# Optimization experiments

Hardware: AMD Instinct MI355X
Metric: run time of the kernel (lower is better)

The kernel has to match this reference:

```python
import jax, jax.numpy as jnp
import numpy as np

B, S, C, DG, DO, G = 128, 512, 256, 256, 4, 10
ZONEOUT = 0.1  # ZoneOutCell eval-mode: h = z*h_prev + (1-z)*h_new


def setup_inputs() -> dict:
    key = jax.random.key(0)
    ks = jax.random.split(key, 12)
    def w(k, shape, fan):
        return jax.random.normal(k, shape, jnp.float32) / np.sqrt(fan).astype(np.float32)
    return {
        "encoder_output": jax.random.normal(ks[0], (B, S, C), jnp.float32),
        "target_prosody": jax.random.normal(ks[1], (B, S, DO), jnp.float32),
        "snt_durations": jax.random.randint(ks[2], (B, S), 0, 10),
        "W_pre": w(ks[3], (DO, DO), DO), "b_pre": jnp.zeros((DO,), jnp.float32),
        "Wih0": w(ks[4], (3 * DG, C + DO), C + DO), "Whh0": w(ks[5], (3 * DG, DG), DG),
        "bih0": jnp.zeros((3 * DG,), jnp.float32), "bhh0": jnp.zeros((3 * DG,), jnp.float32),
        "Wih1": w(ks[6], (3 * DG, DG), DG), "Whh1": w(ks[7], (3 * DG, DG), DG),
        "bih1": jnp.zeros((3 * DG,), jnp.float32), "bhh1": jnp.zeros((3 * DG,), jnp.float32),
        "W_pi": w(ks[8], (G, C + DG), C + DG), "b_pi": jnp.zeros((G,), jnp.float32),
        "W_sigma": w(ks[9], (DO * G, C + DG), C + DG), "b_sigma": jnp.zeros((DO * G,), jnp.float32),
        "W_mu": w(ks[10], (DO * G, C + DG), C + DG), "b_mu": jnp.zeros((DO * G,), jnp.float32),
    }


def _gru_cell(x, h, Wih, Whh, bih, bhh):
    # torch.nn.GRUCell math, wrapped in eval-mode ZoneOut
    gi = x @ Wih.T + bih
    gh = h @ Whh.T + bhh
    ir, iz, inn = jnp.split(gi, 3, axis=-1)
    hr, hz, hn = jnp.split(gh, 3, axis=-1)
    r = jax.nn.sigmoid(ir + hr)
    z = jax.nn.sigmoid(iz + hz)
    n = jnp.tanh(inn + r * hn)
    h_new = (1.0 - z) * n + z * h
    return ZONEOUT * h + (1.0 - ZONEOUT) * h_new


def _forward(encoder_output, target_prosody, W_pre, b_pre, Wih0, Whh0, bih0, bhh0,
             Wih1, Whh1, bih1, bhh1, W_pi, b_pi, W_sigma, b_sigma, W_mu, b_mu):
    tgt = jax.lax.stop_gradient(target_prosody)  # teacher-forced prev_out is detached
    # prev_out at step t is go_frame (zeros) then target[:, t-1]
    prev = jnp.concatenate([jnp.zeros((B, 1, DO), tgt.dtype), tgt[:, :-1, :]], axis=1)
    prenet = prev @ W_pre.T + b_pre                       # (B,S,DO)
    xs = jnp.concatenate([encoder_output, prenet], -1)    # (B,S,C+DO)

    def step(carry, x_t):
        h0, h1 = carry
        h0 = _gru_cell(x_t, h0, Wih0, Whh0, bih0, bhh0)
        h1 = _gru_cell(h0, h1, Wih1, Whh1, bih1, bhh1)
        return (h0, h1), h1

    init = (jnp.zeros((B, DG), xs.dtype), jnp.zeros((B, DG), xs.dtype))
    _, H = jax.lax.scan(step, init, jnp.swapaxes(xs, 0, 1))  # (S,B,DG)
    H = jnp.swapaxes(H, 0, 1)                                # (B,S,DG)

    hcs = jnp.concatenate([H, encoder_output], axis=-1)      # (B,S,DG+C)
    pi = jax.nn.softmax(hcs @ W_pi.T + b_pi, axis=-1)                       # (B,S,G)
    sigma = (jax.nn.elu(hcs @ W_sigma.T + b_sigma) + 1.0).reshape(B, S, G, DO)
    mu = (hcs @ W_mu.T + b_mu).reshape(B, S, G, DO)
    return tgt, pi, sigma, mu


def reference(encoder_output, target_prosody, snt_durations, W_pre, b_pre, Wih0, Whh0,
              bih0, bhh0, Wih1, Whh1, bih1, bhh1, W_pi, b_pi, W_sigma, b_sigma, W_mu, b_mu):
    outs, pi, sigma, mu = _forward(encoder_output, target_prosody, W_pre, b_pre,
                                   Wih0, Whh0, bih0, bhh0, Wih1, Whh1, bih1, bhh1,
                                   W_pi, b_pi, W_sigma, b_sigma, W_mu, b_mu)
    # make_src_mask: True where padded (index >= number of non-zero durations)
    snt_nums = jnp.sum(snt_durations > 0, axis=-1)           # (B,)
    src_snt_mask = jnp.arange(S)[None, :] >= snt_nums[:, None]
    return outs, pi, sigma, mu, src_snt_mask
```

## Files before the change

kernel.cpp:

```cpp
#include <hip/hip_runtime.h>
#include <hip/hip_bf16.h>
#include <stdint.h>

#define B_   128
#define S_   512
#define C_   256
#define DG_  256

#define OFF_PI   262144
#define OFF_SIG  917504
#define OFF_MU   3538944
#define OFF_MASK 6160384

typedef __hip_bfloat16 bf16;
typedef __bf16 bf16x8 __attribute__((ext_vector_type(8)));
typedef float  f32x4  __attribute__((ext_vector_type(4)));
typedef unsigned int u32;
typedef unsigned int u32x4 __attribute__((ext_vector_type(4)));

__device__ __align__(16) bf16  gWmain[768*256];
__device__ __align__(16) bf16  gWHH0 [768*256];
__device__ __align__(16) bf16  gWIH1 [768*256];
__device__ __align__(16) bf16  gWHH1 [768*256];
__device__ __align__(16) bf16  gWcat [96*512];
__device__ __align__(16) float gWtail[768*4];
__device__ __align__(16) float gSm   [3200];
__device__ __align__(16) bf16  gHbuf [B_*S_*DG_];
__device__ __align__(16) bf16  gH0   [B_*S_*DG_];
__device__ __align__(16) float gGi0  [50331648];
__device__ __align__(16) float gGi1  [50331648];
__device__ __align__(16) float gPn   [65536*4];

#define SM_WPRE 0
#define SM_BPRE 16
#define SM_BIH0 20
#define SM_BHH0 788
#define SM_BIH1 1556
#define SM_BHH1 2324
#define SM_BPI  3092
#define SM_BSIG 3102
#define SM_BMU  3142

__device__ __forceinline__ bf16  f2b(float x){ return __float2bfloat16(x); }
__device__ __forceinline__ unsigned short b2u(bf16 x){
    union { bf16 b; unsigned short u; } c; c.b = x; return c.u;
}
__device__ __forceinline__ float sigm(float x){ return 1.f/(1.f + __expf(-x)); }
__device__ __forceinline__ float tanhfast(float x){ return 1.f - 2.f/(__expf(2.f*x) + 1.f); }
__device__ __forceinline__ float rcp_fast(float x){
    float r; asm("v_rcp_f32 %0, %1" : "=v"(r) : "v"(x)); return r;
}
__device__ __forceinline__ u32 cvtpk_bf16(float lo, float hi){
    u32 r; asm("v_cvt_pk_bf16_f32 %0, %1, %2" : "=v"(r) : "v"(lo), "v"(hi)); return r;
}
__device__ __forceinline__ f32x4 mfma16(bf16x8 a, bf16x8 b, f32x4 c){
    return __builtin_amdgcn_mfma_f32_16x16x32_bf16(a, b, c, 0, 0, 0);
}
__device__ __forceinline__ bf16x8 u2b(u32x4 x){
    union { u32x4 u; bf16x8 b; } c; c.u = x; return c.b;
}
__device__ __forceinline__ bf16x8 cvt8(const float* f){
    float4 a = *reinterpret_cast<const float4*>(f);
    float4 c = *reinterpret_cast<const float4*>(f + 4);
    bf16 o[8] = { f2b(a.x),f2b(a.y),f2b(a.z),f2b(a.w),
                  f2b(c.x),f2b(c.y),f2b(c.z),f2b(c.w) };
    return *reinterpret_cast<bf16x8*>(o);
}

#define IN_N0 199680
#define IN_N1 396288
#define IN_N2 592896
#define IN_N3 789504
#define IN_N4 838656
#define IN_N5 841838
#define IN_N6 1103982
__global__ __launch_bounds__(256) void k_ingest(
    const float* __restrict__ Wih0, const float* __restrict__ Whh0,
    const float* __restrict__ Wih1, const float* __restrict__ Whh1,
    const float* __restrict__ Wpi, const float* __restrict__ Wsig,
    const float* __restrict__ Wmu,
    const float* __restrict__ Wpre, const float* __restrict__ bpre,
    const float* __restrict__ bih0, const float* __restrict__ bhh0,
    const float* __restrict__ bih1, const float* __restrict__ bhh1,
    const float* __restrict__ bpi, const float* __restrict__ bsig,
    const float* __restrict__ bmu, const float* __restrict__ tgt)
{
    int j = blockIdx.x*256 + threadIdx.x;
    if (j < IN_N0){
        int r = j/260, c = j - r*260;
        float v = Wih0[j];
        if (c < 256) gWmain[r*256 + c] = f2b(v);
        else         gWtail[r*4 + (c-256)] = v;
    } else if (j < IN_N1){
        int k = j - IN_N0; gWHH0[k] = f2b(Whh0[k]);
    } else if (j < IN_N2){
        int k = j - IN_N1; gWIH1[k] = f2b(Wih1[k]);
    } else if (j < IN_N3){
        int k = j - IN_N2; gWHH1[k] = f2b(Whh1[k]);
    } else if (j < IN_N4){
        int k = j - IN_N3; int r = k >> 9, c = k & 511;
        float v = 0.f;
        if      (r < 10) v = Wpi[r*512 + c];
        else if (r < 50) v = Wsig[(r-10)*512 + c];
        else if (r < 90) v = Wmu[(r-50)*512 + c];
        gWcat[k] = f2b(v);
    } else if (j < IN_N5){
        int k = j - IN_N4;
        float v;
        if      (k < 16)   v = Wpre[k];
        else if (k < 20)   v = bpre[k-16];
        else if (k < 788)  v = bih0[k-20];
        else if (k < 1556) v = bhh0[k-788];
        else if (k < 2324) v = bih1[k-1556];
        else if (k < 3092) v = bhh1[k-2324];
        else if (k < 3102) v = bpi[k-3092];
        else if (k < 3142) v = bsig[k-3102];
        else               v = bmu[k-3142];
        gSm[k] = v;
    } else if (j < IN_N6){
        int k = j - IN_N5, m = k>>2, jj = k&3, tq = m&511;
        float acc = bpre[jj];
        if (tq){
            const float* pv = tgt + (size_t)(m-1)*4;
            #pragma unroll
            for (int q=0;q<4;q++) acc += Wpre[jj*4+q]*pv[q];
        }
        gPn[m*4+jj] = acc;
    }
}

__global__ __launch_bounds__(256) void k_gi0(const float* __restrict__ enc)
{
    const int tid = threadIdx.x, w = tid>>6, lane = tid&63;
    const int col = lane&15, quad = lane>>4;
    const int m0 = blockIdx.x*64 + w*16;

    bf16x8 aF[8];
    #pragma unroll
    for (int kt=0; kt<8; kt++)
        aF[kt] = cvt8(enc + (size_t)(m0+col)*256 + kt*32 + quad*8);

    float4 pnr[4];
    #pragma unroll
    for (int r=0; r<4; r++)
        pnr[r] = *reinterpret_cast<const float4*>(gPn + (size_t)(m0 + quad*4 + r)*4);
    const int mrow = m0 + quad*4;

    for (int nt=0; nt<48; nt++){
        const int n = nt*16 + col;
        f32x4 acc = {0.f,0.f,0.f,0.f};
        #pragma unroll
        for (int kt=0; kt<8; kt++){
            bf16x8 bW = *reinterpret_cast<const bf16x8*>(gWmain + (size_t)n*256 + kt*32 + quad*8);
            acc = mfma16(aF[kt], bW, acc);
        }
        float4 wt = ((const float4*)gWtail)[n];
        float  bi = gSm[SM_BIH0 + n] + ((n < 512) ? gSm[SM_BHH0 + n] : 0.f);
        #pragma unroll
        for (int r=0; r<4; r++){
            int m = mrow + r; int bq = m>>9, tq = m&511;
            float v = acc[r] + bi + wt.x*pnr[r].x + wt.y*pnr[r].y
                              + wt.z*pnr[r].z + wt.w*pnr[r].w;
            gGi0[((size_t)tq*128 + bq)*768 + n] = v;
        }
    }
}

__global__ __launch_bounds__(256) void k_gi1()
{
    const int tid = threadIdx.x, w = tid>>6, lane = tid&63;
    const int col = lane&15, quad = lane>>4;
    const int m0 = blockIdx.x*64 + w*16;

    bf16x8 aF[8];
    #pragma unroll
    for (int kt=0; kt<8; kt++)
        aF[kt] = *reinterpret_cast<const bf16x8*>(gH0 + (size_t)(m0+col)*256 + kt*32 + quad*8);

    for (int nt=0; nt<48; nt++){
        const int n = nt*16 + col;
        f32x4 acc = {0.f,0.f,0.f,0.f};
        #pragma unroll
        for (int kt=0; kt<8; kt++){
            bf16x8 bW = *reinterpret_cast<const bf16x8*>(gWIH1 + (size_t)n*256 + kt*32 + quad*8);
            acc = mfma16(aF[kt], bW, acc);
        }
        float bi = gSm[SM_BIH1 + n] + ((n < 512) ? gSm[SM_BHH1 + n] : 0.f);
        #pragma unroll
        for (int r=0; r<4; r++)
            gGi1[((size_t)(m0 + quad*4 + r))*768 + n] = acc[r] + bi;
    }
}

__global__ __launch_bounds__(256, 1) void k_rec(int layer)
{
    __shared__ bf16 hv[2][4][272];

    const bf16*  __restrict__ W  = layer ? gWHH1 : gWHH0;
    const float* __restrict__ gi = layer ? gGi1  : gGi0;
    const int smOff = layer ? SM_BHH1 : SM_BHH0;
    bf16* __restrict__ hout = layer ? gHbuf : gH0;

    const int tid = threadIdx.x, w = tid>>6, lane = tid&63;
    const int col = lane&15, quad = lane>>4;
    const int bg4 = blockIdx.x*4;
    const int c4 = col&3, qsel = col>>2;

    for (int i=tid; i<2*4*272; i+=256) (&hv[0][0][0])[i] = f2b(0.f);

    u32x4 wA[8][8];
    #pragma unroll
    for (int j=0;j<8;j++){
        const int qi = j/3, g = j - qi*3;
        const bf16* Wr = W + ((size_t)(g*256 + (4*w+qi)*16 + col))*256;
        #pragma unroll
        for (int kt=0;kt<8;kt++){
            wA[j][kt] = *reinterpret_cast<const u32x4*>(Wr + kt*32 + quad*8);
            asm volatile("" : "+a"(wA[j][kt]));
        }
    }
    u32x4 wV[4][8];
    #pragma unroll
    for (int j=0;j<4;j++){
        const int jj = 8+j, qi = jj/3, g = jj - qi*3;
        const bf16* Wr = W + ((size_t)(g*256 + (4*w+qi)*16 + col))*256;
        #pragma unroll
        for (int kt=0;kt<8;kt++){
            wV[j][kt] = *reinterpret_cast<const u32x4*>(Wr + kt*32 + quad*8);
            asm volatile("" : "+v"(wV[j][kt]));
        }
    }

    const int q = 4*w + qsel;
    const int d = q*16 + quad*4;
    float4 bhn = *reinterpret_cast<const float4*>(&gSm[smOff + 512 + d]);
    const float* gib = gi + (size_t)(bg4 + c4)*768 + d;
    bf16* hop; size_t hstep;
    if (layer){ hop = hout + ((size_t)(bg4+c4)*512)*256 + d; hstep = 256; }
    else      { hop = hout + (size_t)(bg4+c4)*256 + d;       hstep = 128*256; }
    float hreg[4] = {0.f,0.f,0.f,0.f};

    float4 gr = *reinterpret_cast<const float4*>(gib);
    float4 gz = *reinterpret_cast<const float4*>(gib + 256);
    float4 gn = *reinterpret_cast<const float4*>(gib + 512);

    __syncthreads();

    #pragma unroll 1
    for (int t=0; t<S_; t++){
        float4 pr, pz, pnx;
        if (t+1 < S_){
            const float* gq = gib + (size_t)(t+1)*98304;
            pr  = *reinterpret_cast<const float4*>(gq);
            pz  = *reinterpret_cast<const float4*>(gq + 256);
            pnx = *reinterpret_cast<const float4*>(gq + 512);
        }

        f32x4 acc[12];
        #pragma unroll
        for (int j=0;j<12;j++) acc[j] = f32x4{0.f,0.f,0.f,0.f};
        asm volatile("s_nop 2" :::);

        const bf16* hrow = &hv[t&1][c4][0];
        #pragma unroll
        for (int kt=0;kt<8;kt++){
            u32x4 hbu = *reinterpret_cast<const u32x4*>(hrow + kt*32 + quad*8);
            #pragma unroll
            for (int j=0;j<8;j++)
                asm volatile("v_mfma_f32_16x16x32_bf16 %0, %1, %2, %0"
                             : "+v"(acc[j]) : "a"(wA[j][kt]), "v"(hbu));
            bf16x8 hbb = u2b(hbu);
            #pragma unroll
            for (int j=0;j<4;j++)
                acc[8+j] = mfma16(u2b(wV[j][kt]), hbb, acc[8+j]);
        }
        asm volatile("s_nop 7\n\ts_nop 7" :::);

        f32x4 aR = (qsel==0) ? acc[0] : (qsel==1) ? acc[3] : (qsel==2) ? acc[6] : acc[9];
        f32x4 aZ = (qsel==0) ? acc[1] : (qsel==1) ? acc[4] : (qsel==2) ? acc[7] : acc[10];
        f32x4 aN = (qsel==0) ? acc[2] : (qsel==1) ? acc[5] : (qsel==2) ? acc[8] : acc[11];

        float hp[4];
        #pragma unroll
        for (int r=0;r<4;r++){
            float rr = rcp_fast(1.f + __expf(-(((const float*)&gr)[r] + aR[r])));
            float zz = rcp_fast(1.f + __expf(-(((const float*)&gz)[r] + aZ[r])));
            float xn = ((const float*)&gn)[r] + rr*(aN[r] + ((const float*)&bhn)[r]);
            float nn = 1.f - 2.f*rcp_fast(__expf(2.f*xn) + 1.f);
            float h  = hreg[r];
            float v  = 0.1f*h + 0.9f*((1.f-zz)*nn + zz*h);
            hreg[r] = v; hp[r] = v;
        }

        uint2 u;
        u.x = cvtpk_bf16(hp[0], hp[1]);
        u.y = cvtpk_bf16(hp[2], hp[3]);
        *reinterpret_cast<uint2*>(&hv[(t&1)^1][c4][d]) = u;
        *reinterpret_cast<uint2*>(hop) = u;  hop += hstep;

        gr = pr; gz = pz; gn = pnx;

        asm volatile("s_waitcnt lgkmcnt(0)" ::: "memory");
        __builtin_amdgcn_sched_barrier(0);
        __builtin_amdgcn_s_barrier();
        __builtin_amdgcn_sched_barrier(0);
    }
}

__global__ __launch_bounds__(256) void k_proj(
    const float* __restrict__ enc, float* __restrict__ dout)
{
    __shared__ float st[128][100];
    const int tid = threadIdx.x, w = tid>>6, lane = tid&63;
    const int col = lane&15, quad = lane>>4;
    const int Mb = blockIdx.x*128;
    const int M0 = Mb + w*32;

    f32x4 acc[2][6];
    #pragma unroll
    for (int mt=0; mt<2; mt++)
        #pragma unroll
        for (int nt=0; nt<6; nt++) acc[mt][nt] = f32x4{0.f,0.f,0.f,0.f};

    #pragma unroll
    for (int kt=0; kt<16; kt++){
        bf16x8 a0, a1;
        if (kt < 8){
            a0 = *reinterpret_cast<const bf16x8*>(gHbuf + (size_t)(M0 +      col)*DG_ + kt*32 + quad*8);
            a1 = *reinterpret_cast<const bf16x8*>(gHbuf + (size_t)(M0 + 16 + col)*DG_ + kt*32 + quad*8);
        } else {
            a0 = cvt8(enc + (size_t)(M0 +      col)*C_ + (kt-8)*32 + quad*8);
            a1 = cvt8(enc + (size_t)(M0 + 16 + col)*C_ + (kt-8)*32 + quad*8);
        }
        #pragma unroll
        for (int nt=0; nt<6; nt++){
            bf16x8 b = *reinterpret_cast<const bf16x8*>(gWcat + (size_t)(nt*16 + col)*512 + kt*32 + quad*8);
            acc[0][nt] = mfma16(a0, b, acc[0][nt]);
            acc[1][nt] = mfma16(a1, b, acc[1][nt]);
        }
    }
    #pragma unroll
    for (int nt=0; nt<6; nt++)
        #pragma unroll
        for (int mt=0; mt<2; mt++)
            #pragma unroll
            for (int r=0; r<4; r++)
                st[w*32 + mt*16 + quad*4 + r][nt*16 + col] = acc[mt][nt][r];
    __syncthreads();

    if (tid < 128){
        const float* v = st[tid];
        const size_t m = (size_t)Mb + tid;
        float x[10], mx = -1e30f;
        #pragma unroll
        for (int g=0; g<10; g++){ x[g] = v[g] + gSm[SM_BPI+g]; mx = fmaxf(mx, x[g]); }
        float sum = 0.f;
        #pragma unroll
        for (int g=0; g<10; g++){ x[g] = __expf(x[g]-mx); sum += x[g]; }
        float inv = 1.f/sum;
        #pragma unroll
        for (int g=0; g<10; g++)
            dout[OFF_PI + m*10 + g] = x[g]*inv;
        #pragma unroll
        for (int i=0; i<40; i++){
            float s = v[10+i] + gSm[SM_BSIG+i];
            dout[OFF_SIG + m*40 + i] = (s > 0.f) ? (s + 1.f) : __expf(s);
        }
        #pragma unroll
        for (int i=0; i<40; i++)
            dout[OFF_MU + m*40 + i] = v[50+i] + gSm[SM_BMU+i];
    }
}

__global__ __launch_bounds__(256) void k_misc(const float* __restrict__ tgt,
    const int* __restrict__ dur, float* __restrict__ dout)
{
    if (blockIdx.x < 256){
        int i = blockIdx.x*256 + threadIdx.x;
        ((float4*)dout)[i] = ((const float4*)tgt)[i];
    } else {
        __shared__ int red[256];
        int b = blockIdx.x - 256;
        int c = 0;
        for (int s = threadIdx.x; s < S_; s += 256) c += (dur[b*S_ + s] > 0) ? 1 : 0;
        red[threadIdx.x] = c;
        __syncthreads();
        for (int off=128; off>0; off>>=1){
            if (threadIdx.x < off) red[threadIdx.x] += red[threadIdx.x+off];
            __syncthreads();
        }
        int snt = red[0];
        for (int s = threadIdx.x; s < S_; s += 256)
            dout[OFF_MASK + (size_t)b*S_ + s] = (s >= snt) ? 1.f : 0.f;
    }
}

extern "C" void kernel_launch(void* const* d_in, const int* in_sizes, int n_in,
                              void* d_out, int out_size, void* d_ws, size_t ws_size,
                              hipStream_t stream)
{
    (void)d_ws; (void)ws_size;
    const float* enc  = (const float*)d_in[0];
    const float* tgt  = (const float*)d_in[1];
    const int*   dur  = (const int*)  d_in[2];
    const float* Wpre = (const float*)d_in[3];
    const float* bpre = (const float*)d_in[4];
    const float* Wih0 = (const float*)d_in[5];
    const float* Whh0 = (const float*)d_in[6];
    const float* bih0 = (const float*)d_in[7];
    const float* bhh0 = (const float*)d_in[8];
    const float* Wih1 = (const float*)d_in[9];
    const float* Whh1 = (const float*)d_in[10];
    const float* bih1 = (const float*)d_in[11];
    const float* bhh1 = (const float*)d_in[12];
    const float* Wpi  = (const float*)d_in[13];
    const float* bpi  = (const float*)d_in[14];
    const float* Wsig = (const float*)d_in[15];
    const float* bsig = (const float*)d_in[16];
    const float* Wmu  = (const float*)d_in[17];
    const float* bmu  = (const float*)d_in[18];
    float* dout = (float*)d_out;

    hipLaunchKernelGGL(k_ingest, dim3(4313), dim3(256), 0, stream,
                       Wih0, Whh0, Wih1, Whh1, Wpi, Wsig, Wmu,
                       Wpre, bpre, bih0, bhh0, bih1, bhh1, bpi, bsig, bmu, tgt);
    hipLaunchKernelGGL(k_gi0,  dim3(1024), dim3(256), 0, stream, enc);
    hipLaunchKernelGGL(k_rec,  dim3(32),   dim3(256), 0, stream, 0);
    hipLaunchKernelGGL(k_gi1,  dim3(1024), dim3(256), 0, stream);
    hipLaunchKernelGGL(k_rec,  dim3(32),   dim3(256), 0, stream, 1);
    hipLaunchKernelGGL(k_proj, dim3(512),  dim3(256), 0, stream, enc, dout);
    hipLaunchKernelGGL(k_misc, dim3(384),  dim3(256), 0, stream, tgt, dur, dout);
}
```

Baseline: 1.982 ms.

## Split recurrent GRU kernel across 8 waves with LDS-staged weight tiles

The recurrent kernel now runs 512 threads (8 waves) per block instead of 4, so each wave owns 2 hidden-dim tiles instead of 4 and issues 6 MFMA chains per k-step instead of 12. Five weight tiles stay in AGPRs and the sixth (n-gate of the second tile) is staged once in LDS and reloaded every step. Each lane now finalizes 2 hidden elements instead of 4. The aim is to shorten the serial per-step critical path, at the cost of a larger barrier across 8 waves and extra LDS traffic each step.

```diff
diff --git a/kernel.cpp b/kernel.cpp
--- a/kernel.cpp
+++ b/kernel.cpp
@@ -46,7 +46,6 @@
     union { bf16 b; unsigned short u; } c; c.b = x; return c.u;
 }
 __device__ __forceinline__ float sigm(float x){ return 1.f/(1.f + __expf(-x)); }
-__device__ __forceinline__ float tanhfast(float x){ return 1.f - 2.f/(__expf(2.f*x) + 1.f); }
 __device__ __forceinline__ float rcp_fast(float x){
     float r; asm("v_rcp_f32 %0, %1" : "=v"(r) : "v"(x)); return r;
 }
@@ -192,8 +191,9 @@
     }
 }
 
-__global__ __launch_bounds__(256, 1) void k_rec(int layer)
-{
+__global__ __launch_bounds__(512, 2) void k_rec(int layer)
+{
+    __shared__ bf16 sW[8][8][64][8];
     __shared__ bf16 hv[2][4][272];
 
     const bf16*  __restrict__ W  = layer ? gWHH1 : gWHH0;
@@ -204,61 +204,59 @@
     const int tid = threadIdx.x, w = tid>>6, lane = tid&63;
     const int col = lane&15, quad = lane>>4;
     const int bg4 = blockIdx.x*4;
-    const int c4 = col&3, qsel = col>>2;
-
-    for (int i=tid; i<2*4*272; i+=256) (&hv[0][0][0])[i] = f2b(0.f);
-
-    u32x4 wA[8][8];
-    #pragma unroll
-    for (int j=0;j<8;j++){
-        const int qi = j/3, g = j - qi*3;
-        const bf16* Wr = W + ((size_t)(g*256 + (4*w+qi)*16 + col))*256;
+
+    for (int i=tid; i<2*4*272; i+=512) (&hv[0][0][0])[i] = f2b(0.f);
+
+    u32x4 wA[5][8];
+    #pragma unroll
+    for (int j=0;j<5;j++){
+        const int g  = (j<3) ? j : (j-3);
+        const int qi = (j<3) ? 0 : 1;
+        const bf16* Wr = W + ((size_t)(g*256 + (2*w+qi)*16 + col))*256;
         #pragma unroll
         for (int kt=0;kt<8;kt++){
             wA[j][kt] = *reinterpret_cast<const u32x4*>(Wr + kt*32 + quad*8);
             asm volatile("" : "+a"(wA[j][kt]));
         }
     }
-    u32x4 wV[4][8];
-    #pragma unroll
-    for (int j=0;j<4;j++){
-        const int jj = 8+j, qi = jj/3, g = jj - qi*3;
-        const bf16* Wr = W + ((size_t)(g*256 + (4*w+qi)*16 + col))*256;
-        #pragma unroll
-        for (int kt=0;kt<8;kt++){
-            wV[j][kt] = *reinterpret_cast<const u32x4*>(Wr + kt*32 + quad*8);
-            asm volatile("" : "+v"(wV[j][kt]));
-        }
-    }
-
-    const int q = 4*w + qsel;
-    const int d = q*16 + quad*4;
-    float4 bhn = *reinterpret_cast<const float4*>(&gSm[smOff + 512 + d]);
+    {
+        const bf16* Wr = W + ((size_t)(2*256 + (2*w+1)*16 + col))*256;
+        #pragma unroll
+        for (int kt=0;kt<8;kt++)
+            *reinterpret_cast<bf16x8*>(&sW[w][kt][lane][0]) =
+                *reinterpret_cast<const bf16x8*>(Wr + kt*32 + quad*8);
+    }
+
+    const int c4 = col&3, qi = (col>>2)&1, sub = col>>3;
+    const int q = 2*w + qi;
+    const int d = q*16 + quad*4 + sub*2;
+    float2 bhn = *reinterpret_cast<const float2*>(&gSm[smOff + 512 + d]);
     const float* gib = gi + (size_t)(bg4 + c4)*768 + d;
     bf16* hop; size_t hstep;
     if (layer){ hop = hout + ((size_t)(bg4+c4)*512)*256 + d; hstep = 256; }
     else      { hop = hout + (size_t)(bg4+c4)*256 + d;       hstep = 128*256; }
-    float hreg[4] = {0.f,0.f,0.f,0.f};
-
-    float4 gr = *reinterpret_cast<const float4*>(gib);
-    float4 gz = *reinterpret_cast<const float4*>(gib + 256);
-    float4 gn = *reinterpret_cast<const float4*>(gib + 512);
+    float h0 = 0.f, h1 = 0.f;
+
+    float2 gr = *reinterpret_cast<const float2*>(gib);
+    float2 gz = *reinterpret_cast<const float2*>(gib + 256);
+    float2 gn = *reinterpret_cast<const float2*>(gib + 512);
 
     __syncthreads();
 
     #pragma unroll 1
     for (int t=0; t<S_; t++){
-        float4 pr, pz, pnx;
+        float2 pr, pz, pn2;
         if (t+1 < S_){
             const float* gq = gib + (size_t)(t+1)*98304;
-            pr  = *reinterpret_cast<const float4*>(gq);
-            pz  = *reinterpret_cast<const float4*>(gq + 256);
-            pnx = *reinterpret_cast<const float4*>(gq + 512);
-        }
-
-        f32x4 acc[12];
-        #pragma unroll
-        for (int j=0;j<12;j++) acc[j] = f32x4{0.f,0.f,0.f,0.f};
+            pr  = *reinterpret_cast<const float2*>(gq);
+            pz  = *reinterpret_cast<const float2*>(gq + 256);
+            pn2 = *reinterpret_cast<const float2*>(gq + 512);
+        }
+        __builtin_amdgcn_sched_barrier(0);
+
+        f32x4 acc[6];
+        #pragma unroll
+        for (int j=0;j<6;j++) acc[j] = f32x4{0.f,0.f,0.f,0.f};
         asm volatile("s_nop 2" :::);
 
         const bf16* hrow = &hv[t&1][c4][0];
@@ -266,39 +264,39 @@
         for (int kt=0;kt<8;kt++){
             u32x4 hbu = *reinterpret_cast<const u32x4*>(hrow + kt*32 + quad*8);
             #pragma unroll
-            for (int j=0;j<8;j++)
+            for (int j=0;j<5;j++)
                 asm volatile("v_mfma_f32_16x16x32_bf16 %0, %1, %2, %0"
                              : "+v"(acc[j]) : "a"(wA[j][kt]), "v"(hbu));
-            bf16x8 hbb = u2b(hbu);
-            #pragma unroll
-            for (int j=0;j<4;j++)
-                acc[8+j] = mfma16(u2b(wV[j][kt]), hbb, acc[8+j]);
+            bf16x8 s5 = *reinterpret_cast<const bf16x8*>(&sW[w][kt][lane][0]);
+            acc[5] = mfma16(s5, u2b(hbu), acc[5]);
         }
         asm volatile("s_nop 7\n\ts_nop 7" :::);
 
-        f32x4 aR = (qsel==0) ? acc[0] : (qsel==1) ? acc[3] : (qsel==2) ? acc[6] : acc[9];
-        f32x4 aZ = (qsel==0) ? acc[1] : (qsel==1) ? acc[4] : (qsel==2) ? acc[7] : acc[10];
-        f32x4 aN = (qsel==0) ? acc[2] : (qsel==1) ? acc[5] : (qsel==2) ? acc[8] : acc[11];
-
-        float hp[4];
-        #pragma unroll
-        for (int r=0;r<4;r++){
-            float rr = rcp_fast(1.f + __expf(-(((const float*)&gr)[r] + aR[r])));
-            float zz = rcp_fast(1.f + __expf(-(((const float*)&gz)[r] + aZ[r])));
-            float xn = ((const float*)&gn)[r] + rr*(aN[r] + ((const float*)&bhn)[r]);
-            float nn = 1.f - 2.f*rcp_fast(__expf(2.f*xn) + 1.f);
-            float h  = hreg[r];
-            float v  = 0.1f*h + 0.9f*((1.f-zz)*nn + zz*h);
-            hreg[r] = v; hp[r] = v;
-        }
-
-        uint2 u;
-        u.x = cvtpk_bf16(hp[0], hp[1]);
-        u.y = cvtpk_bf16(hp[2], hp[3]);
-        *reinterpret_cast<uint2*>(&hv[(t&1)^1][c4][d]) = u;
-        *reinterpret_cast<uint2*>(hop) = u;  hop += hstep;
-
-        gr = pr; gz = pz; gn = pnx;
+        f32x4 aR = qi ? acc[3] : acc[0];
+        f32x4 aZ = qi ? acc[4] : acc[1];
+        f32x4 aN = qi ? acc[5] : acc[2];
+        float ar0 = sub ? aR[2] : aR[0], ar1 = sub ? aR[3] : aR[1];
+        float az0 = sub ? aZ[2] : aZ[0], az1 = sub ? aZ[3] : aZ[1];
+        float an0 = sub ? aN[2] : aN[0], an1 = sub ? aN[3] : aN[1];
+
+        float rr0 = rcp_fast(1.f + __expf(-(gr.x + ar0)));
+        float zz0 = rcp_fast(1.f + __expf(-(gz.x + az0)));
+        float xn0 = gn.x + rr0*(an0 + bhn.x);
+        float nn0 = 1.f - 2.f*rcp_fast(__expf(2.f*xn0) + 1.f);
+        float v0  = 0.1f*h0 + 0.9f*((1.f-zz0)*nn0 + zz0*h0);
+        h0 = v0;
+        float rr1 = rcp_fast(1.f + __expf(-(gr.y + ar1)));
+        float zz1 = rcp_fast(1.f + __expf(-(gz.y + az1)));
+        float xn1 = gn.y + rr1*(an1 + bhn.y);
+        float nn1 = 1.f - 2.f*rcp_fast(__expf(2.f*xn1) + 1.f);
+        float v1  = 0.1f*h1 + 0.9f*((1.f-zz1)*nn1 + zz1*h1);
+        h1 = v1;
+
+        u32 u = cvtpk_bf16(v0, v1);
+        *reinterpret_cast<u32*>(&hv[(t&1)^1][c4][d]) = u;
+        *reinterpret_cast<u32*>(hop) = u;  hop += hstep;
+
+        gr = pr; gz = pz; gn = pn2;
 
         asm volatile("s_waitcnt lgkmcnt(0)" ::: "memory");
         __builtin_amdgcn_sched_barrier(0);
@@ -425,9 +423,9 @@
                        Wih0, Whh0, Wih1, Whh1, Wpi, Wsig, Wmu,
                        Wpre, bpre, bih0, bhh0, bih1, bhh1, bpi, bsig, bmu, tgt);
     hipLaunchKernelGGL(k_gi0,  dim3(1024), dim3(256), 0, stream, enc);
-    hipLaunchKernelGGL(k_rec,  dim3(32),   dim3(256), 0, stream, 0);
+    hipLaunchKernelGGL(k_rec,  dim3(32),   dim3(512), 0, stream, 0);
     hipLaunchKernelGGL(k_gi1,  dim3(1024), dim3(256), 0, stream);
-    hipLaunchKernelGGL(k_rec,  dim3(32),   dim3(256), 0, stream, 1);
+    hipLaunchKernelGGL(k_rec,  dim3(32),   dim3(512), 0, stream, 1);
     hipLaunchKernelGGL(k_proj, dim3(512),  dim3(256), 0, stream, enc, dout);
     hipLaunchKernelGGL(k_misc, dim3(384),  dim3(256), 0, stream, tgt, dur, dout);
 }
```

New measurement: 1.859 ms. -6.2%, faster.
